# Kernel optimization log

Measured on AMD Instinct MI355X. Metric: run time of the kernel, lower is better.

## Reference

```python
import jax, jax.numpy as jnp
import numpy as np

EPS = float(np.finfo(np.float32).eps)
QMIN, QMAX = -128, 127


def setup_inputs() -> dict:
    key = jax.random.key(0)
    k_x, k_w, k_ws, k_b = jax.random.split(key, 4)
    M, K, N = 32768, 1024, 1024
    x = jax.random.normal(k_x, (M, K), dtype=jnp.float32)
    # per-channel symmetrically quantized, transposed weight: [K, N], values in [-128, 127]
    w_int8_t = jax.random.randint(k_w, (K, N), QMIN, QMAX + 1, dtype=jnp.int32).astype(jnp.int8)
    # per-out-channel scales (positive, float; torch uses float64, we use float32)
    w_scales = (jax.random.uniform(k_ws, (N,), dtype=jnp.float32) * 0.02 + 1e-4)
    # preprocessed column sums: w_int8_t.sum(dim=0)
    w_int8_t_sums = w_int8_t.astype(jnp.int32).sum(axis=0)
    bias = jax.random.normal(k_b, (N,), dtype=jnp.float32)
    return {
        "x": x,
        "w_int8_t": w_int8_t,
        "w_scales": w_scales,
        "w_int8_t_sums": w_int8_t_sums,
        "bias": bias,
    }


def reference(x, w_int8_t, w_scales, w_int8_t_sums, bias):
    # ---- dynamically_quantize_per_tensor (affine, int8) ----
    min_neg = jnp.minimum(jnp.min(x), jnp.float32(0.0))
    max_pos = jnp.maximum(jnp.max(x), jnp.float32(0.0))
    x_scale = jnp.maximum((max_pos - min_neg) / jnp.float32(QMAX - QMIN), EPS)
    x_zp = jnp.clip(QMIN - jnp.round(min_neg / x_scale), QMIN, QMAX)  # scalar
    x_q = jnp.clip(jnp.round(x / x_scale) + x_zp, QMIN, QMAX).astype(jnp.int8)

    # ---- int8 matmul with int32 accumulation (safe_int_mm equivalent) ----
    xw_i32 = jnp.matmul(
        x_q.astype(jnp.int32), w_int8_t.astype(jnp.int32)
    )  # [M, N] int32

    # ---- dequant with zero-point correction (quant_int8_matmul) ----
    mm_unscaled = xw_i32.astype(jnp.float32) - x_zp * w_int8_t_sums.astype(jnp.float32)
    y = x_scale * w_scales * mm_unscaled  # broadcast w_scales over N

    # ---- bias add (quant_int8_dynamic_linear) ----
    y = y + bias
    return y.astype(jnp.float32)
```

## Files before the change

kernel.cpp:

```cpp
#include <hip/hip_runtime.h>
#include <stdint.h>

#define M_DIM 32768
#define K_DIM 1024
#define N_DIM 1024

typedef int v4i __attribute__((ext_vector_type(4)));

__device__ __forceinline__ void gld_lds16(const void* g, void* lds) {
    __builtin_amdgcn_global_load_lds(
        (const __attribute__((address_space(1))) unsigned int*)g,
        (__attribute__((address_space(3))) unsigned int*)lds, 16, 0, 0);
}

__global__ void k_minmax(const float* __restrict__ x,
                         float* __restrict__ pmin, float* __restrict__ pmax) {
    int t = threadIdx.x;
    long gid = (long)blockIdx.x * blockDim.x + t;
    const float4* x4 = (const float4*)x;
    const long n4 = (long)M_DIM * K_DIM / 4;
    float mn = INFINITY, mx = -INFINITY;
    for (long i = gid; i < n4; i += (long)gridDim.x * blockDim.x) {
        float4 v = x4[i];
        mn = fminf(mn, fminf(fminf(v.x, v.y), fminf(v.z, v.w)));
        mx = fmaxf(mx, fmaxf(fmaxf(v.x, v.y), fmaxf(v.z, v.w)));
    }
    __shared__ float smn[256], smx[256];
    smn[t] = mn; smx[t] = mx;
    __syncthreads();
    for (int s = 128; s > 0; s >>= 1) {
        if (t < s) {
            smn[t] = fminf(smn[t], smn[t + s]);
            smx[t] = fmaxf(smx[t], smx[t + s]);
        }
        __syncthreads();
    }
    if (t == 0) { pmin[blockIdx.x] = smn[0]; pmax[blockIdx.x] = smx[0]; }
}

__global__ void k_finalize(const float* __restrict__ pmin,
                           const float* __restrict__ pmax,
                           float* __restrict__ sp) {
    int t = threadIdx.x;
    float mn = INFINITY, mx = -INFINITY;
    for (int i = t; i < 1024; i += 256) {
        mn = fminf(mn, pmin[i]);
        mx = fmaxf(mx, pmax[i]);
    }
    __shared__ float smn[256], smx[256];
    smn[t] = mn; smx[t] = mx;
    __syncthreads();
    for (int s = 128; s > 0; s >>= 1) {
        if (t < s) {
            smn[t] = fminf(smn[t], smn[t + s]);
            smx[t] = fmaxf(smx[t], smx[t + s]);
        }
        __syncthreads();
    }
    if (t == 0) {
        float min_neg = fminf(smn[0], 0.0f);
        float max_pos = fmaxf(smx[0], 0.0f);
        float scale = (max_pos - min_neg) / 255.0f;
        scale = fmaxf(scale, 1.1920928955078125e-07f);
        float zp = -128.0f - rintf(min_neg / scale);
        zp = fminf(fmaxf(zp, -128.0f), 127.0f);
        sp[0] = scale;
        sp[1] = zp;
    }
}

__device__ __forceinline__ unsigned q4(float4 v, float s, float zp) {
    int a = (int)fminf(fmaxf(rintf(v.x / s) + zp, -128.0f), 127.0f);
    int b = (int)fminf(fmaxf(rintf(v.y / s) + zp, -128.0f), 127.0f);
    int c = (int)fminf(fmaxf(rintf(v.z / s) + zp, -128.0f), 127.0f);
    int d = (int)fminf(fmaxf(rintf(v.w / s) + zp, -128.0f), 127.0f);
    return (a & 255) | ((b & 255) << 8) | ((c & 255) << 16) | ((d & 255) << 24);
}

__global__ void k_quant(const float* __restrict__ x,
                        const float* __restrict__ sp,
                        int8_t* __restrict__ xq) {
    float s = sp[0], zp = sp[1];
    long g = (long)blockIdx.x * blockDim.x + threadIdx.x;
    const float4* x4 = (const float4*)x + g * 4;
    float4 v0 = x4[0], v1 = x4[1], v2 = x4[2], v3 = x4[3];
    uint4 r;
    r.x = q4(v0, s, zp);
    r.y = q4(v1, s, zp);
    r.z = q4(v2, s, zp);
    r.w = q4(v3, s, zp);
    ((uint4*)xq)[g] = r;
}

__global__ void k_transpose(const int* __restrict__ w, int8_t* __restrict__ wt) {
    __shared__ int8_t tile[32][33];
    int bn = blockIdx.x * 32;
    int bk = blockIdx.y * 32;
    int tx = threadIdx.x, ty = threadIdx.y;
#pragma unroll
    for (int i = 0; i < 32; i += 8)
        tile[ty + i][tx] = (int8_t)w[(long)(bk + ty + i) * N_DIM + bn + tx];
    __syncthreads();
#pragma unroll
    for (int i = 0; i < 32; i += 8)
        wt[(long)(bn + ty + i) * K_DIM + bk + tx] = tile[tx][ty + i];
}

__global__ __launch_bounds__(256) void k_gemm(
    const int8_t* __restrict__ xq, const int8_t* __restrict__ wt,
    const float* __restrict__ sp, const float* __restrict__ w_scales,
    const int* __restrict__ wsums, const float* __restrict__ bias,
    float* __restrict__ out) {
    __shared__ __align__(16) int8_t lds_a[128 * 64];
    __shared__ __align__(16) int8_t lds_b[128 * 64];

    const int t = threadIdx.x;
    const int m0 = blockIdx.y * 128;
    const int n0 = blockIdx.x * 128;
    const int w = t >> 6, l = t & 63, quad = l >> 4, r = l & 15;
    const int wave_m = (w & 1) * 64, wave_n = (w >> 1) * 64;

    v4i acc[4][4];
#pragma unroll
    for (int i = 0; i < 4; i++)
#pragma unroll
        for (int j = 0; j < 4; j++) acc[i][j] = (v4i){0, 0, 0, 0};

    const int slot0 = t, slot1 = 256 + t;
    const int row0 = slot0 >> 2, s0 = slot0 & 3;
    const int row1 = slot1 >> 2, s1 = slot1 & 3;
    const int q0 = s0 ^ (row0 & 3) ^ ((row0 >> 2) & 3);
    const int q1 = s1 ^ (row1 & 3) ^ ((row1 >> 2) & 3);
    const int8_t* gA0 = xq + (long)(m0 + row0) * K_DIM + q0 * 16;
    const int8_t* gA1 = xq + (long)(m0 + row1) * K_DIM + q1 * 16;
    const int8_t* gB0 = wt + (long)(n0 + row0) * K_DIM + q0 * 16;
    const int8_t* gB1 = wt + (long)(n0 + row1) * K_DIM + q1 * 16;

    int ra[4], rb[4];
#pragma unroll
    for (int i = 0; i < 4; i++) {
        int mrow = wave_m + i * 16 + r;
        int sa = quad ^ (mrow & 3) ^ ((mrow >> 2) & 3);
        ra[i] = mrow * 64 + sa * 16;
        int nrow = wave_n + i * 16 + r;
        int sb = quad ^ (nrow & 3) ^ ((nrow >> 2) & 3);
        rb[i] = nrow * 64 + sb * 16;
    }

    for (int kb = 0; kb < K_DIM; kb += 64) {
        gld_lds16(gA0 + kb, lds_a + slot0 * 16);
        gld_lds16(gA1 + kb, lds_a + slot1 * 16);
        gld_lds16(gB0 + kb, lds_b + slot0 * 16);
        gld_lds16(gB1 + kb, lds_b + slot1 * 16);
        __syncthreads();

        v4i af[4], bf[4];
#pragma unroll
        for (int i = 0; i < 4; i++) af[i] = *(const v4i*)(lds_a + ra[i]);
#pragma unroll
        for (int j = 0; j < 4; j++) bf[j] = *(const v4i*)(lds_b + rb[j]);
#pragma unroll
        for (int i = 0; i < 4; i++)
#pragma unroll
            for (int j = 0; j < 4; j++)
                acc[i][j] = __builtin_amdgcn_mfma_i32_16x16x64_i8(af[i], bf[j], acc[i][j], 0, 0, 0);
        __syncthreads();
    }

    const float scale = sp[0], zp = sp[1];
#pragma unroll
    for (int j = 0; j < 4; j++) {
        int n = n0 + wave_n + j * 16 + r;
        float sj = scale * w_scales[n];
        float cj = zp * (float)wsums[n];
        float bj = bias[n];
#pragma unroll
        for (int i = 0; i < 4; i++) {
            int mbase = m0 + wave_m + i * 16 + quad * 4;
#pragma unroll
            for (int e = 0; e < 4; e++) {
                out[(long)(mbase + e) * N_DIM + n] = sj * ((float)acc[i][j][e] - cj) + bj;
            }
        }
    }
}

extern "C" void kernel_launch(void* const* d_in, const int* in_sizes, int n_in,
                              void* d_out, int out_size, void* d_ws, size_t ws_size,
                              hipStream_t stream) {
    const float* x        = (const float*)d_in[0];
    const int*   w_int8_t = (const int*)d_in[1];
    const float* w_scales = (const float*)d_in[2];
    const int*   w_sums   = (const int*)d_in[3];
    const float* bias     = (const float*)d_in[4];
    float* out = (float*)d_out;

    float* wsf  = (float*)d_ws;
    float* pmin = wsf;
    float* pmax = wsf + 1024;
    float* sp   = wsf + 2048;
    int8_t* wt  = (int8_t*)d_ws + 16384;
    int8_t* xq  = (int8_t*)d_ws + 16384 + (size_t)K_DIM * N_DIM;

    k_minmax<<<1024, 256, 0, stream>>>(x, pmin, pmax);
    k_finalize<<<1, 256, 0, stream>>>(pmin, pmax, sp);
    k_quant<<<8192, 256, 0, stream>>>(x, sp, xq);
    k_transpose<<<dim3(N_DIM / 32, K_DIM / 32), dim3(32, 8), 0, stream>>>(w_int8_t, wt);
    k_gemm<<<dim3(N_DIM / 128, M_DIM / 128), 256, 0, stream>>>(
        xq, wt, sp, w_scales, w_sums, bias, out);
}
```

Baseline: 318.6 us.

## Double-buffer GEMM LDS, remap blocks per XCD, coalesce quant, widen minmax grid

The GEMM now uses two LDS buffers so global-to-LDS loads for the next K tile are issued while MFMAs consume the current one. It also switches to a 1D grid with an XCD-aware mapping so blocks on the same die share M rows and W columns in L2. The quant kernel now uses grid-strided float4 loads so each access is coalesced, and the minmax pass runs twice as many blocks with matching workspace offsets. Doubling LDS use may reduce occupancy.

```diff
diff --git a/kernel.cpp b/kernel.cpp
--- a/kernel.cpp
+++ b/kernel.cpp
@@ -43,7 +43,7 @@
                            float* __restrict__ sp) {
     int t = threadIdx.x;
     float mn = INFINITY, mx = -INFINITY;
-    for (int i = t; i < 1024; i += 256) {
+    for (int i = t; i < 2048; i += 256) {
         mn = fminf(mn, pmin[i]);
         mx = fmaxf(mx, pmax[i]);
     }
@@ -81,15 +81,18 @@
                         const float* __restrict__ sp,
                         int8_t* __restrict__ xq) {
     float s = sp[0], zp = sp[1];
+    const long stride = (long)gridDim.x * blockDim.x;
     long g = (long)blockIdx.x * blockDim.x + threadIdx.x;
-    const float4* x4 = (const float4*)x + g * 4;
-    float4 v0 = x4[0], v1 = x4[1], v2 = x4[2], v3 = x4[3];
-    uint4 r;
-    r.x = q4(v0, s, zp);
-    r.y = q4(v1, s, zp);
-    r.z = q4(v2, s, zp);
-    r.w = q4(v3, s, zp);
-    ((uint4*)xq)[g] = r;
+    const float4* x4 = (const float4*)x;
+    unsigned* xq4 = (unsigned*)xq;
+    float4 v0 = x4[g];
+    float4 v1 = x4[g + stride];
+    float4 v2 = x4[g + 2 * stride];
+    float4 v3 = x4[g + 3 * stride];
+    xq4[g]              = q4(v0, s, zp);
+    xq4[g + stride]     = q4(v1, s, zp);
+    xq4[g + 2 * stride] = q4(v2, s, zp);
+    xq4[g + 3 * stride] = q4(v3, s, zp);
 }
 
 __global__ void k_transpose(const int* __restrict__ w, int8_t* __restrict__ wt) {
@@ -111,12 +114,16 @@
     const float* __restrict__ sp, const float* __restrict__ w_scales,
     const int* __restrict__ wsums, const float* __restrict__ bias,
     float* __restrict__ out) {
-    __shared__ __align__(16) int8_t lds_a[128 * 64];
-    __shared__ __align__(16) int8_t lds_b[128 * 64];
+    __shared__ __align__(16) int8_t lds_a[2][128 * 64];
+    __shared__ __align__(16) int8_t lds_b[2][128 * 64];
+
+    const int b = blockIdx.x;
+    const int xcd = b & 7;
+    const int s = b >> 3;
+    const int n0 = (s & 7) * 128;
+    const int m0 = (xcd * 32 + (s >> 3)) * 128;
 
     const int t = threadIdx.x;
-    const int m0 = blockIdx.y * 128;
-    const int n0 = blockIdx.x * 128;
     const int w = t >> 6, l = t & 63, quad = l >> 4, r = l & 15;
     const int wave_m = (w & 1) * 64, wave_n = (w >> 1) * 64;
 
@@ -140,32 +147,44 @@
 #pragma unroll
     for (int i = 0; i < 4; i++) {
         int mrow = wave_m + i * 16 + r;
-        int sa = quad ^ (mrow & 3) ^ ((mrow >> 2) & 3);
-        ra[i] = mrow * 64 + sa * 16;
+        ra[i] = mrow * 64 + (quad ^ (mrow & 3) ^ ((mrow >> 2) & 3)) * 16;
         int nrow = wave_n + i * 16 + r;
-        int sb = quad ^ (nrow & 3) ^ ((nrow >> 2) & 3);
-        rb[i] = nrow * 64 + sb * 16;
-    }
-
-    for (int kb = 0; kb < K_DIM; kb += 64) {
-        gld_lds16(gA0 + kb, lds_a + slot0 * 16);
-        gld_lds16(gA1 + kb, lds_a + slot1 * 16);
-        gld_lds16(gB0 + kb, lds_b + slot0 * 16);
-        gld_lds16(gB1 + kb, lds_b + slot1 * 16);
-        __syncthreads();
-
-        v4i af[4], bf[4];
-#pragma unroll
-        for (int i = 0; i < 4; i++) af[i] = *(const v4i*)(lds_a + ra[i]);
-#pragma unroll
-        for (int j = 0; j < 4; j++) bf[j] = *(const v4i*)(lds_b + rb[j]);
-#pragma unroll
-        for (int i = 0; i < 4; i++)
-#pragma unroll
-            for (int j = 0; j < 4; j++)
-                acc[i][j] = __builtin_amdgcn_mfma_i32_16x16x64_i8(af[i], bf[j], acc[i][j], 0, 0, 0);
-        __syncthreads();
-    }
+        rb[i] = nrow * 64 + (quad ^ (nrow & 3) ^ ((nrow >> 2) & 3)) * 16;
+    }
+
+#define STAGE(buf, kb)                                        \
+    do {                                                      \
+        gld_lds16(gA0 + (kb) * 64, lds_a[buf] + slot0 * 16);  \
+        gld_lds16(gA1 + (kb) * 64, lds_a[buf] + slot1 * 16);  \
+        gld_lds16(gB0 + (kb) * 64, lds_b[buf] + slot0 * 16);  \
+        gld_lds16(gB1 + (kb) * 64, lds_b[buf] + slot1 * 16);  \
+    } while (0)
+
+#define CONSUME(buf)                                                         \
+    do {                                                                     \
+        v4i af[4], bf[4];                                                    \
+        _Pragma("unroll") for (int i = 0; i < 4; i++)                        \
+            af[i] = *(const v4i*)(lds_a[buf] + ra[i]);                       \
+        _Pragma("unroll") for (int j = 0; j < 4; j++)                        \
+            bf[j] = *(const v4i*)(lds_b[buf] + rb[j]);                       \
+        _Pragma("unroll") for (int i = 0; i < 4; i++)                        \
+            _Pragma("unroll") for (int j = 0; j < 4; j++)                    \
+                acc[i][j] = __builtin_amdgcn_mfma_i32_16x16x64_i8(           \
+                    af[i], bf[j], acc[i][j], 0, 0, 0);                       \
+    } while (0)
+
+    STAGE(0, 0);
+#pragma unroll
+    for (int kb = 0; kb < 16; kb += 2) {
+        __syncthreads();
+        if (kb + 1 < 16) STAGE(1, kb + 1);
+        CONSUME(0);
+        __syncthreads();
+        if (kb + 2 < 16) STAGE(0, kb + 2);
+        CONSUME(1);
+    }
+#undef STAGE
+#undef CONSUME
 
     const float scale = sp[0], zp = sp[1];
 #pragma unroll
@@ -197,15 +216,14 @@
 
     float* wsf  = (float*)d_ws;
     float* pmin = wsf;
-    float* pmax = wsf + 1024;
-    float* sp   = wsf + 2048;
-    int8_t* wt  = (int8_t*)d_ws + 16384;
-    int8_t* xq  = (int8_t*)d_ws + 16384 + (size_t)K_DIM * N_DIM;
-
-    k_minmax<<<1024, 256, 0, stream>>>(x, pmin, pmax);
+    float* pmax = wsf + 2048;
+    float* sp   = wsf + 4096;
+    int8_t* wt  = (int8_t*)d_ws + 32768;
+    int8_t* xq  = (int8_t*)d_ws + 32768 + (size_t)K_DIM * N_DIM;
+
+    k_minmax<<<2048, 256, 0, stream>>>(x, pmin, pmax);
     k_finalize<<<1, 256, 0, stream>>>(pmin, pmax, sp);
     k_quant<<<8192, 256, 0, stream>>>(x, sp, xq);
     k_transpose<<<dim3(N_DIM / 32, K_DIM / 32), dim3(32, 8), 0, stream>>>(w_int8_t, wt);
-    k_gemm<<<dim3(N_DIM / 128, M_DIM / 128), 256, 0, stream>>>(
-        xq, wt, sp, w_scales, w_sums, bias, out);
-}
+    k_gemm<<<2048, 256, 0, stream>>>(xq, wt, sp, w_scales, w_sums, bias, out);
+}
```

Result: no change. 322.9 us (+1.3%).
